# Performance work log

Hardware: AMD Instinct MI355X
Metric: run time of the kernel (lower is better)

The kernel has to match this reference:

```python
import jax, jax.numpy as jnp
import numpy as np

# LIDIA core constants (arch_opt.rgb=True => patch_w=5, k=14)
PS = 5          # patch width
K = 14          # number of nearest neighbors
WS = 15         # spatial search window (forward default is 29; 15 keeps working set in ridge regime)
SW = WS // 2    # search radius
PW = PS // 2    # patch radius
RAD = SW + PW   # total reflect pad


def setup_inputs() -> dict:
    key = jax.random.key(0)
    noisy = jax.random.uniform(key, (4, 3, 128, 128), dtype=jnp.float32) * 255.0
    sigma = jnp.full((1,), 25.0, dtype=jnp.float32)  # noise std on 0-255 scale
    return {"noisy": noisy, "sigma": sigma}


def reference(noisy, sigma):
    t, c, h, w = noisy.shape
    # rescale to [-1,1] and remove per-frame means (as in forward)
    x = (noisy / 255.0 - 0.5) / 0.5
    means = x.mean((-2, -1), keepdims=True)
    x = x - means

    # reflect pad so every search offset + patch stays in bounds
    P = jnp.pad(x, ((0, 0), (0, 0), (RAD, RAD), (RAD, RAD)), mode="reflect")
    Hp, Wp = h + 2 * PW, w + 2 * PW
    base = P[:, :, SW:SW + Hp, SW:SW + Wp]  # [t,c,Hp,Wp]

    # --- patch-kNN search: L2 patch distance for every offset in WSxWS window ---
    offs = jnp.stack(jnp.meshgrid(jnp.arange(WS), jnp.arange(WS), indexing="ij"),
                     axis=-1).reshape(-1, 2)  # [WS*WS, 2]

    def energy(o):
        sh = jax.lax.dynamic_slice(P, (0, 0, o[0], o[1]), (t, c, Hp, Wp))
        return ((base - sh) ** 2).sum(1)  # [t,Hp,Wp]

    E = jax.vmap(energy)(offs)  # [WS*WS, t, Hp, Wp] pixel-wise sq diffs

    # box-filter (PSxPS patch sum) -> per-center patch distances
    ones_k = jnp.ones((1, 1, PS, PS), dtype=E.dtype)
    D = jax.lax.conv_general_dilated(E.reshape(-1, 1, Hp, Wp), ones_k,
                                     window_strides=(1, 1), padding="VALID")
    D = D.reshape(WS * WS, t, h, w).transpose(1, 2, 3, 0)  # [t,h,w,WS*WS]

    # top-k smallest distances per query pixel
    negD, idx = jax.lax.top_k(-D, K)  # [t,h,w,K]
    topd = -negD
    oy = idx // WS  # offset row in [0,WS)
    ox = idx % WS

    # --- gather neighbor patches (irregular gather) ---
    # patch top-left in padded coords: row = i + oy  (RAD - SW - PW == 0)
    ii = jnp.arange(h)[None, :, None, None]
    jj = jnp.arange(w)[None, None, :, None]
    r0 = ii + oy  # [t,h,w,K]
    c0 = jj + ox
    a = jnp.arange(PS)
    rows = r0[..., None, None] + a[None, None, None, None, :, None]  # [t,h,w,K,PS,1]
    cols = c0[..., None, None] + a[None, None, None, None, None, :]  # [t,h,w,K,1,PS]
    tt = jnp.arange(t)[:, None, None, None, None, None]
    Pt = P.transpose(0, 2, 3, 1)  # [t,Hpad,Wpad,c]
    patches = Pt[tt, rows, cols]  # [t,h,w,K,PS,PS,c]

    # --- denoise: distance-based softmax aggregation over neighbors ---
    sig = sigma[0] / 255.0 / 0.5  # noise std in normalized units
    denom = 2.0 * (c * PS * PS) * (sig * sig) + 1e-8
    wts = jax.nn.softmax(-topd / denom, axis=-1)  # [t,h,w,K]
    deno_p = jnp.einsum("thwk,thwkpqc->thwpqc", wts, patches)  # [t,h,w,PS,PS,c]

    # --- fold: scatter-add overlapping denoised patches + counts ---
    rf = (jnp.arange(h)[:, None, None, None] + a[None, None, :, None])  # [h,1,PS,1]
    cf = (jnp.arange(w)[None, :, None, None] + a[None, None, None, :])  # [1,w,1,PS]
    tf = jnp.arange(t)[:, None, None, None, None]
    acc = jnp.zeros((t, Hp, Wp, c), dtype=deno_p.dtype)
    cnt = jnp.zeros((t, Hp, Wp, 1), dtype=deno_p.dtype)
    acc = acc.at[tf, rf[None], cf[None]].add(deno_p)
    cnt = cnt.at[tf, rf[None], cf[None]].add(
        jnp.ones((t, h, w, PS, PS, 1), dtype=deno_p.dtype))

    deno = acc / (cnt + 1e-10)
    deno = deno[:, PW:PW + h, PW:PW + w, :].transpose(0, 3, 1, 2)  # [t,c,h,w]
    deno = deno + means
    deno = 255.0 * (deno * 0.5 + 0.5)
    return deno
```

## Files before the change

kernel.cpp:

```cpp
#include <hip/hip_runtime.h>

#define T_ 4
#define C_ 3
#define H_ 128
#define W_ 128
#define PS_ 5
#define K_ 14
#define WS_ 15
#define SW_ 7
#define PW_ 2
#define RAD_ 9
#define HP_ 146
#define NOFF 225
#define NPIX (T_*H_*W_)
#define NQ 2

#define TILE 16
#define SPR 34
#define SPS 35
#define SSR 30
#define SSS 33
#define OB 12
#define NB 10
#define CSOG 324
#define CSBUF (OB*CSOG)
#define VOG 256
#define VBUF (OB*VOG)

#define AT 8
#define APR 22
#define APS 23
#define AWR 12
#define AWS 20

typedef unsigned int u32;

__device__ __forceinline__ float4 load_refl(const float* __restrict__ noisy,
                                            int t, int py, int px) {
    int ry = py - RAD_; if (ry < 0) ry = -ry; if (ry > H_-1) ry = 2*(H_-1) - ry;
    int rx = px - RAD_; if (rx < 0) rx = -rx; if (rx > W_-1) rx = 2*(W_-1) - rx;
    const float* nt = noisy + (size_t)t*(C_*H_*W_) + ry*W_ + rx;
    float4 v;
    v.x = nt[0]          * (1.0f/127.5f) - 1.0f;
    v.y = nt[H_*W_]      * (1.0f/127.5f) - 1.0f;
    v.z = nt[2*(H_*W_)]  * (1.0f/127.5f) - 1.0f;
    v.w = 0.f;
    return v;
}

__device__ __forceinline__ void batch_of(int q, int bi, int& ob, int& len) {
    if (q == 0) { int oi = NB-1 - bi; ob = oi*OB; len = (oi == NB-1) ? 5 : OB; }
    else        { ob = 113 + bi*OB;   len = (bi == NB-1) ? 4 : OB; }
}

__global__ __launch_bounds__(512, 4) void fused_topk(const float* __restrict__ noisy,
                                                     uint4* __restrict__ pkey) {
    __shared__ __align__(16) float4 sP[SPR*SPS];
    __shared__ __align__(16) float  sS[SSR*SSS];
    __shared__ __align__(16) float  cs[2*CSBUF];
    __shared__ __align__(16) float  vb[2*VBUF];

    const int tid = threadIdx.x;
    const int pix = tid & 255;
    const int part = tid >> 8;
    const int tx = pix & 15, ty = pix >> 4;
    const int z = blockIdx.z;
    const int t = z >> 1, q = z & 1;
    const int i0 = blockIdx.y * TILE, j0 = blockIdx.x * TILE;

    {
        float* qsq = cs;
        for (int e = tid; e < SPR*SPR; e += 512) {
            int r = e / SPR, c = e % SPR;
            float4 v = load_refl(noisy, t, i0 + r, j0 + c);
            sP[r*SPS + c] = v;
            qsq[r*35 + c] = v.x*v.x + v.y*v.y + v.z*v.z;
        }
    }
    __syncthreads();

    {
        const float* qsq = cs;
        float* cq  = cs + 1200;
        for (int e = tid; e < 30*34; e += 512) {
            int r = e / 34, c = e - r*34;
            const float* qp = &qsq[r*35 + c];
            cq[r*35 + c] = qp[0] + qp[35] + qp[70] + qp[105] + qp[140];
        }
        __syncthreads();
        for (int e = tid; e < 30*30; e += 512) {
            int r = e / 30, c = e - r*30;
            const float* cp = &cq[r*35 + c];
            sS[r*SSS + c] = cp[0] + cp[1] + cp[2] + cp[3] + cp[4];
        }
        __syncthreads();
    }

    const float Sbase = sS[(ty + SW_)*SSS + (tx + SW_)];

    const int og = tid / 20;
    const int cc = tid - og*20;
    const bool p1thr = (tid < OB*20);
    float bx[20], by[20], bz[20];
    if (p1thr) {
        #pragma unroll
        for (int r = 0; r < 20; ++r) {
            float4 v = sP[(SW_ + r)*SPS + (cc + SW_)];
            bx[r] = v.x; by[r] = v.y; bz[r] = v.z;
        }
    }

    const int t2 = tid - 256;
    const bool p2thr = (t2 >= 0 && t2 < OB*16);
    const int p2g = p2thr ? (t2 >> 4) : 0;
    const int p2i = t2 & 15;

    u32 kb[K_];
    #pragma unroll
    for (int k = 0; k < K_; ++k) kb[k] = 0xFFFFFFFFu;

    for (int i = 0; i <= NB + 1; ++i) {
        if (i < NB && p1thr) {
            int ob, len; batch_of(q, i, ob, len);
            if (og < len) {
                int o = ob + og;
                u32 oyu = (u32)o / 15u, oxu = (u32)o - oyu*15u;
                const float4* sp = &sP[(int)oyu*SPS + cc + (int)oxu];
                float* myv = &cs[(i & 1)*CSBUF + og*CSOG + cc];
                float ring[5]; float run = 0.f;
                #pragma unroll
                for (int r = 0; r < 20; ++r) {
                    float4 sv = sp[r*SPS];
                    float hr = bx[r]*sv.x + by[r]*sv.y + bz[r]*sv.z;
                    if (r < 5) run += hr;
                    else       run += hr - ring[r % 5];
                    ring[r % 5] = hr;
                    if (r >= 4) myv[(r-4)*20] = run;
                }
            }
        }
        if (i >= 1 && i <= NB && p2thr) {
            int ob, len; batch_of(q, i - 1, ob, len);
            if (p2g < len) {
                const float* p2row = &cs[((i-1) & 1)*CSBUF + p2g*CSOG + p2i*20];
                float* vout = &vb[((i-1) & 1)*VBUF + p2g*VOG + p2i*16];
                float4 A = *(const float4*)(p2row);
                float4 B = *(const float4*)(p2row + 4);
                float4 Cv = *(const float4*)(p2row + 8);
                float4 Dv = *(const float4*)(p2row + 12);
                float4 Ev = *(const float4*)(p2row + 16);
                float v0=A.x,v1=A.y,v2=A.z,v3=A.w,v4=B.x,v5=B.y,v6=B.z,v7=B.w;
                float v8=Cv.x,v9=Cv.y,v10=Cv.z,v11=Cv.w,v12=Dv.x,v13=Dv.y,v14=Dv.z,v15=Dv.w;
                float v16=Ev.x,v17=Ev.y,v18=Ev.z,v19=Ev.w;
                float r0 = v0+v1+v2+v3+v4;
                float r1 = r0 + v5 - v0;
                float r2 = r1 + v6 - v1;
                float r3 = r2 + v7 - v2;
                float r4 = r3 + v8 - v3;
                float r5 = r4 + v9 - v4;
                float r6 = r5 + v10 - v5;
                float r7 = r6 + v11 - v6;
                float r8 = r7 + v12 - v7;
                float r9 = r8 + v13 - v8;
                float r10 = r9 + v14 - v9;
                float r11 = r10 + v15 - v10;
                float r12 = r11 + v16 - v11;
                float r13 = r12 + v17 - v12;
                float r14 = r13 + v18 - v13;
                float r15 = r14 + v19 - v14;
                *(float4*)(vout)      = make_float4(r0, r1, r2, r3);
                *(float4*)(vout + 4)  = make_float4(r4, r5, r6, r7);
                *(float4*)(vout + 8)  = make_float4(r8, r9, r10, r11);
                *(float4*)(vout + 12) = make_float4(r12, r13, r14, r15);
            }
        }
        if (i >= 2) {
            int ob, len; batch_of(q, i - 2, ob, len);
            const float* vbase = &vb[((i-2) & 1)*VBUF + pix];
            for (int g = part; g < len; g += 2) {
                int o2 = ob + g;
                u32 oy2 = (u32)o2 / 15u, ox2 = (u32)o2 - oy2*15u;
                float V = vbase[g*VOG];
                float d = fmaxf(Sbase + sS[(ty + (int)oy2)*SSS + (tx + (int)ox2)] - 2.f*V, 0.f);
                u32 c = (__float_as_uint(d) & 0xFFFFFF00u) | (u32)o2;
                #pragma unroll
                for (int k = K_-1; k > 0; --k) kb[k] = min(kb[k], max(kb[k-1], c));
                kb[0] = min(kb[0], c);
            }
        }
        __syncthreads();
    }

    if (part == 1) {
        u32* ex = (u32*)cs + pix*20;
        *(uint4*)(ex)      = make_uint4(kb[0],  kb[1],  kb[2],  kb[3]);
        *(uint4*)(ex + 4)  = make_uint4(kb[4],  kb[5],  kb[6],  kb[7]);
        *(uint4*)(ex + 8)  = make_uint4(kb[8],  kb[9],  kb[10], kb[11]);
        *(uint4*)(ex + 12) = make_uint4(kb[12], kb[13], 0xFFFFFFFFu, 0xFFFFFFFFu);
    }
    __syncthreads();
    if (part == 0) {
        const u32* ex = (const u32*)cs + pix*20;
        uint4 e0 = *(const uint4*)(ex);
        uint4 e1 = *(const uint4*)(ex + 4);
        uint4 e2 = *(const uint4*)(ex + 8);
        uint4 e3 = *(const uint4*)(ex + 12);
        u32 A[16] = {kb[0],kb[1],kb[2],kb[3],kb[4],kb[5],kb[6],kb[7],
                     kb[8],kb[9],kb[10],kb[11],kb[12],kb[13],0xFFFFFFFFu,0xFFFFFFFFu};
        u32 B[16] = {e0.x,e0.y,e0.z,e0.w, e1.x,e1.y,e1.z,e1.w,
                     e2.x,e2.y,e2.z,e2.w, e3.x,e3.y,e3.z,e3.w};
        #pragma unroll
        for (int i2 = 0; i2 < 16; ++i2) A[i2] = min(A[i2], B[15 - i2]);
        #define CEX(x,y) { u32 mn = min(A[x],A[y]); u32 mx = max(A[x],A[y]); A[x]=mn; A[y]=mx; }
        CEX(0,8) CEX(1,9) CEX(2,10) CEX(3,11) CEX(4,12) CEX(5,13) CEX(6,14) CEX(7,15)
        CEX(0,4) CEX(1,5) CEX(2,6) CEX(3,7) CEX(8,12) CEX(9,13) CEX(10,14) CEX(11,15)
        CEX(0,2) CEX(1,3) CEX(4,6) CEX(5,7) CEX(8,10) CEX(9,11) CEX(12,14) CEX(13,15)
        CEX(0,1) CEX(2,3) CEX(4,5) CEX(6,7) CEX(8,9) CEX(10,11) CEX(12,13) CEX(14,15)
        #undef CEX
        int px = ((t*H_ + i0 + ty)*W_ + j0 + tx);
        uint4* pk = pkey + ((size_t)q*NPIX + px)*4;
        pk[0] = make_uint4(A[0],  A[1],  A[2],  A[3]);
        pk[1] = make_uint4(A[4],  A[5],  A[6],  A[7]);
        pk[2] = make_uint4(A[8],  A[9],  A[10], A[11]);
        pk[3] = make_uint4(A[12], A[13], A[14], A[15]);
    }
}

__global__ __launch_bounds__(256, 4) void agg_kernel(const float* __restrict__ noisy,
                                                     const uint4* __restrict__ pkey,
                                                     const float* __restrict__ sigma,
                                                     float* __restrict__ out) {
    __shared__ float sPx[APR*APS];
    __shared__ float sPy[APR*APS];
    __shared__ float sPz[APR*APS];
    __shared__ float sWt[AWR*AWR*AWS];
    __shared__ uint4 sIx[AWR*AWR];

    const int tid = threadIdx.x;
    const int part = tid & 3;
    const int lp = tid >> 2;
    const int tx = lp & 7, ty = lp >> 3;
    const int i0 = blockIdx.y * AT, j0 = blockIdx.x * AT;
    const int t = blockIdx.z;

    for (int e = tid; e < APR*APR; e += 256) {
        int r = e / APR, c = e - r*APR;
        float4 v = load_refl(noisy, t, i0 + 2 + r, j0 + 2 + c);
        sPx[r*APS + c] = v.x;
        sPy[r*APS + c] = v.y;
        sPz[r*APS + c] = v.z;
    }

    if (tid < AWR*AWR) {
        int r = tid / AWR, c = tid - r*AWR;
        int qi = i0 - 2 + r, qj = j0 - 2 + c;
        if (qi >= 0 && qi < H_ && qj >= 0 && qj < W_) {
            size_t px = ((size_t)t*H_ + qi)*W_ + qj;
            u32 A[16];
            {
                const uint4* pk = pkey + px*4;
                uint4 a0=pk[0], a1=pk[1], a2=pk[2], a3=pk[3];
                A[0]=a0.x; A[1]=a0.y; A[2]=a0.z; A[3]=a0.w;
                A[4]=a1.x; A[5]=a1.y; A[6]=a1.z; A[7]=a1.w;
                A[8]=a2.x; A[9]=a2.y; A[10]=a2.z; A[11]=a2.w;
                A[12]=a3.x; A[13]=a3.y; A[14]=a3.z; A[15]=a3.w;
            }
            {
                const uint4* pk = pkey + ((size_t)NPIX + px)*4;
                uint4 b0=pk[0], b1=pk[1], b2=pk[2], b3=pk[3];
                u32 B[16] = {b0.x,b0.y,b0.z,b0.w, b1.x,b1.y,b1.z,b1.w,
                             b2.x,b2.y,b2.z,b2.w, b3.x,b3.y,b3.z,b3.w};
                #pragma unroll
                for (int i2 = 0; i2 < 16; ++i2) A[i2] = min(A[i2], B[15 - i2]);
                #define CEX(x,y) { u32 mn = min(A[x],A[y]); u32 mx = max(A[x],A[y]); A[x]=mn; A[y]=mx; }
                CEX(0,8) CEX(1,9) CEX(2,10) CEX(3,11) CEX(4,12) CEX(5,13) CEX(6,14) CEX(7,15)
                CEX(0,4) CEX(1,5) CEX(2,6) CEX(3,7) CEX(8,12) CEX(9,13) CEX(10,14) CEX(11,15)
                CEX(0,2) CEX(1,3) CEX(4,6) CEX(5,7) CEX(8,10) CEX(9,11) CEX(12,14) CEX(13,15)
                CEX(0,1) CEX(2,3) CEX(4,5) CEX(6,7) CEX(8,9) CEX(10,11) CEX(12,13) CEX(14,15)
                #undef CEX
            }
            float sig = sigma[0] * (1.0f/255.0f) * 2.0f;
            float denom = 2.0f * (float)(C_*PS_*PS_) * (sig*sig) + 1e-8f;
            float d0 = __uint_as_float(A[0] & 0xFFFFFF00u);
            float w[K_]; float sum = 0.f;
            #pragma unroll
            for (int k = 0; k < K_; ++k) {
                float d = __uint_as_float(A[k] & 0xFFFFFF00u);
                w[k] = expf(-(d - d0) / denom); sum += w[k];
            }
            float inv = 1.0f / sum;
            float4* dst = (float4*)&sWt[tid*AWS];
            dst[0] = make_float4(w[0]*inv,  w[1]*inv,  w[2]*inv,  w[3]*inv);
            dst[1] = make_float4(w[4]*inv,  w[5]*inv,  w[6]*inv,  w[7]*inv);
            dst[2] = make_float4(w[8]*inv,  w[9]*inv,  w[10]*inv, w[11]*inv);
            dst[3] = make_float4(w[12]*inv, w[13]*inv, 0.f, 0.f);
            u32 db[K_];
            #pragma unroll
            for (int k = 0; k < K_; ++k) {
                u32 o_ = A[k] & 255u;
                u32 dy = o_ / 15u, dx = o_ - dy*15u;
                db[k] = (dy << 4) | dx;
            }
            uint4 iv;
            iv.x = db[0]  | (db[1]<<8)  | (db[2]<<16)  | (db[3]<<24);
            iv.y = db[4]  | (db[5]<<8)  | (db[6]<<16)  | (db[7]<<24);
            iv.z = db[8]  | (db[9]<<8)  | (db[10]<<16) | (db[11]<<24);
            iv.w = db[12] | (db[13]<<8);
            sIx[tid] = iv;
        }
    }
    __syncthreads();

    const int i = i0 + ty, j = j0 + tx;
    float s0 = 0.f, s1 = 0.f, s2 = 0.f;
    for (int ab = part; ab < 25; ab += 4) {
        int a = ab / 5, b = ab % 5;
        int qi = i + PW_ - a, qj = j + PW_ - b;
        if (qi < 0 || qi >= H_ || qj < 0 || qj >= W_) continue;
        int le = (ty + 4 - a)*AWR + (tx + 4 - b);
        const float4* wv = (const float4*)&sWt[le*AWS];
        float4 wa = wv[0], wb = wv[1], wc = wv[2], wd = wv[3];
        uint4 ip = sIx[le];
        #define ACC(wval, bbits) { \
            u32 b_ = (bbits); \
            int li = (ty + (int)(b_ >> 4))*APS + tx + (int)(b_ & 15u); \
            float w_ = (wval); \
            s0 += w_ * sPx[li]; s1 += w_ * sPy[li]; s2 += w_ * sPz[li]; }
        ACC(wa.x, ip.x & 255u);       ACC(wa.y, (ip.x>>8) & 255u);
        ACC(wa.z, (ip.x>>16) & 255u); ACC(wa.w, ip.x>>24);
        ACC(wb.x, ip.y & 255u);       ACC(wb.y, (ip.y>>8) & 255u);
        ACC(wb.z, (ip.y>>16) & 255u); ACC(wb.w, ip.y>>24);
        ACC(wc.x, ip.z & 255u);       ACC(wc.y, (ip.z>>8) & 255u);
        ACC(wc.z, (ip.z>>16) & 255u); ACC(wc.w, ip.z>>24);
        ACC(wd.x, ip.w & 255u);       ACC(wd.y, (ip.w>>8) & 255u);
        #undef ACC
    }

    s0 += __shfl_xor(s0, 1, 64); s0 += __shfl_xor(s0, 2, 64);
    s1 += __shfl_xor(s1, 1, 64); s1 += __shfl_xor(s1, 2, 64);
    s2 += __shfl_xor(s2, 1, 64); s2 += __shfl_xor(s2, 2, 64);

    if (part == 0) {
        int na = min(4, i + 2) - max(0, i - 125) + 1;
        int nb = min(4, j + 2) - max(0, j - 125) + 1;
        float invc = 1.0f / ((float)(na * nb) + 1e-10f);
        size_t obase = (size_t)t*(C_*H_*W_) + (size_t)i*W_ + j;
        out[obase]             = 127.5f * (s0*invc + 1.0f);
        out[obase +   H_*W_]   = 127.5f * (s1*invc + 1.0f);
        out[obase + 2*(H_*W_)] = 127.5f * (s2*invc + 1.0f);
    }
}

extern "C" void kernel_launch(void* const* d_in, const int* in_sizes, int n_in,
                              void* d_out, int out_size, void* d_ws, size_t ws_size,
                              hipStream_t stream) {
    const float* noisy = (const float*)d_in[0];
    const float* sigma = (const float*)d_in[1];
    float* out = (float*)d_out;
    float* ws  = (float*)d_ws;

    uint4* pkey = (uint4*)ws;

    hipLaunchKernelGGL(fused_topk, dim3(W_/TILE, H_/TILE, T_*NQ), dim3(512), 0, stream,
                       noisy, pkey);

    hipLaunchKernelGGL(agg_kernel, dim3(W_/AT, H_/AT, T_), dim3(256), 0, stream,
                       noisy, pkey, sigma, out);
}
```

Baseline: 55.85 us.

## Run top-k insertion on upper half of threads only, drop cross-half merge

The per-pixel top-k insertion was split across both 256-thread halves, each handling alternate offsets, followed by a shared-memory bitonic merge of the two partial lists. Now only threads 256-511 do the insertion for all offsets of each batch and write their list directly, which removes the merge, its extra barrier and its shared-memory traffic. Threads 0-255, which also do the phase-1 correlation work, no longer do insertion, so the per-stage load is rebalanced. The cost is that the insertion phase per batch becomes serial over twice as many offsets per thread.

```diff
diff --git a/kernel.cpp b/kernel.cpp
--- a/kernel.cpp
+++ b/kernel.cpp
@@ -61,9 +61,6 @@
     __shared__ __align__(16) float  vb[2*VBUF];
 
     const int tid = threadIdx.x;
-    const int pix = tid & 255;
-    const int part = tid >> 8;
-    const int tx = pix & 15, ty = pix >> 4;
     const int z = blockIdx.z;
     const int t = z >> 1, q = z & 1;
     const int i0 = blockIdx.y * TILE, j0 = blockIdx.x * TILE;
@@ -95,8 +92,6 @@
         }
         __syncthreads();
     }
-
-    const float Sbase = sS[(ty + SW_)*SSS + (tx + SW_)];
 
     const int og = tid / 20;
     const int cc = tid - og*20;
@@ -114,6 +109,11 @@
     const bool p2thr = (t2 >= 0 && t2 < OB*16);
     const int p2g = p2thr ? (t2 >> 4) : 0;
     const int p2i = t2 & 15;
+
+    const bool p3thr = (tid >= 256);
+    const int pix3 = tid & 255;
+    const int tx3 = pix3 & 15, ty3 = pix3 >> 4;
+    const float Sbase = sS[(ty3 + SW_)*SSS + (tx3 + SW_)];
 
     u32 kb[K_];
     #pragma unroll
@@ -174,14 +174,14 @@
                 *(float4*)(vout + 12) = make_float4(r12, r13, r14, r15);
             }
         }
-        if (i >= 2) {
+        if (i >= 2 && p3thr) {
             int ob, len; batch_of(q, i - 2, ob, len);
-            const float* vbase = &vb[((i-2) & 1)*VBUF + pix];
-            for (int g = part; g < len; g += 2) {
+            const float* vbase = &vb[((i-2) & 1)*VBUF + pix3];
+            for (int g = 0; g < len; ++g) {
                 int o2 = ob + g;
                 u32 oy2 = (u32)o2 / 15u, ox2 = (u32)o2 - oy2*15u;
                 float V = vbase[g*VOG];
-                float d = fmaxf(Sbase + sS[(ty + (int)oy2)*SSS + (tx + (int)ox2)] - 2.f*V, 0.f);
+                float d = fmaxf(Sbase + sS[(ty3 + (int)oy2)*SSS + (tx3 + (int)ox2)] - 2.f*V, 0.f);
                 u32 c = (__float_as_uint(d) & 0xFFFFFF00u) | (u32)o2;
                 #pragma unroll
                 for (int k = K_-1; k > 0; --k) kb[k] = min(kb[k], max(kb[k-1], c));
@@ -191,38 +191,13 @@
         __syncthreads();
     }
 
-    if (part == 1) {
-        u32* ex = (u32*)cs + pix*20;
-        *(uint4*)(ex)      = make_uint4(kb[0],  kb[1],  kb[2],  kb[3]);
-        *(uint4*)(ex + 4)  = make_uint4(kb[4],  kb[5],  kb[6],  kb[7]);
-        *(uint4*)(ex + 8)  = make_uint4(kb[8],  kb[9],  kb[10], kb[11]);
-        *(uint4*)(ex + 12) = make_uint4(kb[12], kb[13], 0xFFFFFFFFu, 0xFFFFFFFFu);
-    }
-    __syncthreads();
-    if (part == 0) {
-        const u32* ex = (const u32*)cs + pix*20;
-        uint4 e0 = *(const uint4*)(ex);
-        uint4 e1 = *(const uint4*)(ex + 4);
-        uint4 e2 = *(const uint4*)(ex + 8);
-        uint4 e3 = *(const uint4*)(ex + 12);
-        u32 A[16] = {kb[0],kb[1],kb[2],kb[3],kb[4],kb[5],kb[6],kb[7],
-                     kb[8],kb[9],kb[10],kb[11],kb[12],kb[13],0xFFFFFFFFu,0xFFFFFFFFu};
-        u32 B[16] = {e0.x,e0.y,e0.z,e0.w, e1.x,e1.y,e1.z,e1.w,
-                     e2.x,e2.y,e2.z,e2.w, e3.x,e3.y,e3.z,e3.w};
-        #pragma unroll
-        for (int i2 = 0; i2 < 16; ++i2) A[i2] = min(A[i2], B[15 - i2]);
-        #define CEX(x,y) { u32 mn = min(A[x],A[y]); u32 mx = max(A[x],A[y]); A[x]=mn; A[y]=mx; }
-        CEX(0,8) CEX(1,9) CEX(2,10) CEX(3,11) CEX(4,12) CEX(5,13) CEX(6,14) CEX(7,15)
-        CEX(0,4) CEX(1,5) CEX(2,6) CEX(3,7) CEX(8,12) CEX(9,13) CEX(10,14) CEX(11,15)
-        CEX(0,2) CEX(1,3) CEX(4,6) CEX(5,7) CEX(8,10) CEX(9,11) CEX(12,14) CEX(13,15)
-        CEX(0,1) CEX(2,3) CEX(4,5) CEX(6,7) CEX(8,9) CEX(10,11) CEX(12,13) CEX(14,15)
-        #undef CEX
-        int px = ((t*H_ + i0 + ty)*W_ + j0 + tx);
+    if (p3thr) {
+        int px = ((t*H_ + i0 + ty3)*W_ + j0 + tx3);
         uint4* pk = pkey + ((size_t)q*NPIX + px)*4;
-        pk[0] = make_uint4(A[0],  A[1],  A[2],  A[3]);
-        pk[1] = make_uint4(A[4],  A[5],  A[6],  A[7]);
-        pk[2] = make_uint4(A[8],  A[9],  A[10], A[11]);
-        pk[3] = make_uint4(A[12], A[13], A[14], A[15]);
+        pk[0] = make_uint4(kb[0],  kb[1],  kb[2],  kb[3]);
+        pk[1] = make_uint4(kb[4],  kb[5],  kb[6],  kb[7]);
+        pk[2] = make_uint4(kb[8],  kb[9],  kb[10], kb[11]);
+        pk[3] = make_uint4(kb[12], kb[13], 0xFFFFFFFFu, 0xFFFFFFFFu);
     }
 }
 
```

New measurement: 54.21 us. 2.9% less time.
